# Optimization experiments

Hardware: AMD Instinct MI355X
Metric: run time of the kernel (lower is better)

Reference implementation:

```python
import jax, jax.numpy as jnp
import numpy as np

NUM_QUBITS = 12
BOND_DIM = 8
DIM = 2 ** NUM_QUBITS  # 4096


def setup_inputs() -> dict:
    key = jax.random.key(0)
    k0, k1, k2, k3 = jax.random.split(key, 4)
    core0 = jax.random.normal(k0, (2, BOND_DIM), dtype=jnp.float32) * 0.5
    cores_mid = jax.random.normal(k1, (NUM_QUBITS - 2, BOND_DIM, 2, BOND_DIM), dtype=jnp.float32) * 0.5
    core_last = jax.random.normal(k2, (BOND_DIM, 2), dtype=jnp.float32) * 0.5
    A = jax.random.normal(k3, (DIM, DIM), dtype=jnp.float32)
    H = 0.5 * (A + A.T)  # Hamiltonians are symmetric
    return {"core0": core0, "cores_mid": cores_mid, "core_last": core_last, "H": H}


def _build_state(core0, cores_mid, core_last):
    # Sequential MPS contraction: state grows (2^k, D) site by site.
    state = core0  # (2, D)
    n_mid = cores_mid.shape[0]
    D = core0.shape[1]
    for i in range(n_mid):  # fixed, small layer loop (not a data-dim loop)
        # (S, a) x (a, p, b) -> (S, p, b) -> (S*2, b)
        state = jnp.einsum('sa,apb->spb', state, cores_mid[i]).reshape(-1, D)
    # (S, a) x (a, p) -> flat state vector of length 2^n
    psi = jnp.einsum('sa,ap->sp', state, core_last).reshape(-1)
    return psi


def reference(core0, cores_mid, core_last, H):
    psi = _build_state(core0, cores_mid, core_last)  # (2^n,)
    norm = jnp.dot(psi, psi)
    hpsi = H @ psi
    energy = jnp.dot(psi, hpsi) / norm          # <psi|H|psi>/<psi|psi>
    e2 = jnp.dot(psi, H @ hpsi) / norm          # <psi|H^2|psi>/<psi|psi>
    variance = jnp.maximum(e2 - energy * energy, 0.0)
    return jnp.stack([energy, variance])
```

## Files before the change

kernel.cpp:

```cpp
#include <hip/hip_runtime.h>
#include <hip/hip_bf16.h>


#define DIM 4096
#define BOND 8
#define NMID 10
#define T 128
#define NT (DIM / T)
#define NPAIRS (NT * (NT + 1) / 2)


__global__ __launch_bounds__(256) void init_kernel(float* __restrict__ hpsi_g,
                                                   int* __restrict__ cnt) {
  const float4 z = {0.f, 0.f, 0.f, 0.f};
  reinterpret_cast<float4*>(hpsi_g)[blockIdx.x * 256 + threadIdx.x] = z;
  if (blockIdx.x == 0 && threadIdx.x == 0) *cnt = 0;
}

__global__ __launch_bounds__(256) void fused_kernel(
    const float* __restrict__ core0,
    const float* __restrict__ cores_mid,
    const float* __restrict__ core_last,
    const float* __restrict__ H,
    float* __restrict__ psi_g,
    float* __restrict__ hpsi_g,
    int* __restrict__ cnt,
    float* __restrict__ out) {
  __shared__ float c0[16], cm[NMID * 128], cl[16];
  __shared__ float xI[T], xJ[T], yI_s[T], yJp[4 * T];
  __shared__ double sred[12];
  __shared__ int s_old;

  int rem = blockIdx.x;
  int bi = 0;
  while (rem >= NT - bi) { rem -= (NT - bi); ++bi; }
  const int bj = bi + rem;
  const bool diag = (bi == bj);

  if (threadIdx.x < 16) {
    c0[threadIdx.x] = core0[threadIdx.x];
    cl[threadIdx.x] = core_last[threadIdx.x];
  }
  for (int j = threadIdx.x; j < NMID * 128; j += 256) cm[j] = cores_mid[j];
  __syncthreads();

  {
    const int local = threadIdx.x & 127;
    const int slice = (threadIdx.x < 128) ? bi : bj;
    const int idx = slice * T + local;

    float v[BOND], nv[BOND];
    const int s0 = (idx >> 11) & 1;
#pragma unroll
    for (int a = 0; a < BOND; a++) v[a] = c0[s0 * BOND + a];
#pragma unroll
    for (int i = 0; i < NMID; i++) {
      const int p = (idx >> (10 - i)) & 1;
      const float* M = &cm[i * 128 + p * BOND];
#pragma unroll
      for (int b = 0; b < BOND; b++) nv[b] = v[0] * M[b];
#pragma unroll
      for (int a = 1; a < BOND; a++) {
#pragma unroll
        for (int b = 0; b < BOND; b++) nv[b] += v[a] * M[a * 16 + b];
      }
#pragma unroll
      for (int a = 0; a < BOND; a++) v[a] = nv[a];
    }
    const int pl = idx & 1;
    float ps = 0.f;
#pragma unroll
    for (int a = 0; a < BOND; a++) ps += v[a] * cl[a * 2 + pl];

    if (threadIdx.x < 128) xI[local] = ps; else xJ[local] = ps;

    if (diag && threadIdx.x < 128) psi_g[idx] = ps;
  }
  __syncthreads();

  const int wave = threadIdx.x >> 6;
  const int lane = threadIdx.x & 63;
  const float* __restrict__ base = H + (size_t)(bi * T) * DIM + bj * T;

  float aJx = 0.f, aJy = 0.f;
  const float pJx = xJ[lane * 2], pJy = xJ[lane * 2 + 1];

#pragma unroll 4
  for (int k = 0; k < T / 4; ++k) {
    const int r = k * 4 + wave;
    const float2 a = *reinterpret_cast<const float2*>(base + (size_t)r * DIM + lane * 2);
    const float xr = xI[r];
    aJx += a.x * xr;
    aJy += a.y * xr;
    float d = a.x * pJx + a.y * pJy;
#pragma unroll
    for (int off = 32; off > 0; off >>= 1) d += __shfl_down(d, off, 64);
    if (lane == 0) yI_s[r] = d;
  }

  yJp[wave * T + lane * 2] = aJx;
  yJp[wave * T + lane * 2 + 1] = aJy;
  __syncthreads();

  if (threadIdx.x < T) {
    atomicAdd(&hpsi_g[bi * T + threadIdx.x], yI_s[threadIdx.x]);
    if (!diag) {
      const float yj = yJp[threadIdx.x] + yJp[T + threadIdx.x] +
                       yJp[2 * T + threadIdx.x] + yJp[3 * T + threadIdx.x];
      atomicAdd(&hpsi_g[bj * T + threadIdx.x], yj);
    }
  }
  __syncthreads();

  if (threadIdx.x == 0) {
    __threadfence();
    s_old = atomicAdd(cnt, 1);
  }
  __syncthreads();
  if (s_old == NPAIRS - 1) {
    __threadfence();
    double n = 0.0, ph = 0.0, hh = 0.0;
    for (int i = threadIdx.x; i < DIM; i += 256) {
      const float p = __hip_atomic_load(&psi_g[i], __ATOMIC_RELAXED,
                                        __HIP_MEMORY_SCOPE_AGENT);
      const float h = __hip_atomic_load(&hpsi_g[i], __ATOMIC_RELAXED,
                                        __HIP_MEMORY_SCOPE_AGENT);
      const double pd = (double)p, hd = (double)h;
      n += pd * pd;
      ph += pd * hd;
      hh += hd * hd;
    }
#pragma unroll
    for (int off = 32; off > 0; off >>= 1) {
      n += __shfl_down(n, off, 64);
      ph += __shfl_down(ph, off, 64);
      hh += __shfl_down(hh, off, 64);
    }
    if (lane == 0) { sred[wave] = n; sred[4 + wave] = ph; sred[8 + wave] = hh; }
    __syncthreads();
    if (threadIdx.x == 0) {
      double N = 0.0, P = 0.0, HH = 0.0;
#pragma unroll
      for (int w = 0; w < 4; w++) { N += sred[w]; P += sred[4 + w]; HH += sred[8 + w]; }
      const double e = P / N;
      const double e2 = HH / N;
      double var = e2 - e * e;
      if (var < 0.0) var = 0.0;
      out[0] = (float)e;
      out[1] = (float)var;
    }
  }
}

extern "C" void kernel_launch(void* const* d_in, const int* in_sizes, int n_in,
                              void* d_out, int out_size, void* d_ws, size_t ws_size,
                              hipStream_t stream) {
  const float* core0 = (const float*)d_in[0];
  const float* cores_mid = (const float*)d_in[1];
  const float* core_last = (const float*)d_in[2];
  const float* H = (const float*)d_in[3];

  float* psi = (float*)d_ws;
  float* hpsi = psi + DIM;
  int* cnt = (int*)(hpsi + DIM);

  init_kernel<<<4, 256, 0, stream>>>(hpsi, cnt);
  fused_kernel<<<NPAIRS, 256, 0, stream>>>(core0, cores_mid, core_last, H,
                                           psi, hpsi, cnt, (float*)d_out);
}
```

Before: 132.6 us.

## Precompute psi in init kernel and widen symv tile loads with LDS row reduction

```diff
diff --git a/kernel.cpp b/kernel.cpp
--- a/kernel.cpp
+++ b/kernel.cpp
@@ -10,24 +10,60 @@
 #define NPAIRS (NT * (NT + 1) / 2)
 
 
-__global__ __launch_bounds__(256) void init_kernel(float* __restrict__ hpsi_g,
-                                                   int* __restrict__ cnt) {
-  const float4 z = {0.f, 0.f, 0.f, 0.f};
-  reinterpret_cast<float4*>(hpsi_g)[blockIdx.x * 256 + threadIdx.x] = z;
-  if (blockIdx.x == 0 && threadIdx.x == 0) *cnt = 0;
-}
-
-__global__ __launch_bounds__(256) void fused_kernel(
+__global__ __launch_bounds__(256) void init_kernel(
     const float* __restrict__ core0,
     const float* __restrict__ cores_mid,
     const float* __restrict__ core_last,
+    float* __restrict__ psi_g,
+    float* __restrict__ hpsi_g,
+    int* __restrict__ cnt) {
+  __shared__ float c0[16], cm[NMID * 128], cl[16];
+
+  if (threadIdx.x < 16) {
+    c0[threadIdx.x] = core0[threadIdx.x];
+    cl[threadIdx.x] = core_last[threadIdx.x];
+  }
+  for (int j = threadIdx.x; j < NMID * 128; j += 256) cm[j] = cores_mid[j];
+  __syncthreads();
+
+  const int idx = blockIdx.x * 256 + threadIdx.x;
+  hpsi_g[idx] = 0.f;
+  if (idx == 0) *cnt = 0;
+
+  float v[BOND], nv[BOND];
+  const int s0 = (idx >> 11) & 1;
+#pragma unroll
+  for (int a = 0; a < BOND; a++) v[a] = c0[s0 * BOND + a];
+#pragma unroll
+  for (int i = 0; i < NMID; i++) {
+    const int p = (idx >> (10 - i)) & 1;
+    const float* M = &cm[i * 128 + p * BOND];
+#pragma unroll
+    for (int b = 0; b < BOND; b++) nv[b] = v[0] * M[b];
+#pragma unroll
+    for (int a = 1; a < BOND; a++) {
+#pragma unroll
+      for (int b = 0; b < BOND; b++) nv[b] += v[a] * M[a * 16 + b];
+    }
+#pragma unroll
+    for (int a = 0; a < BOND; a++) v[a] = nv[a];
+  }
+  const int pl = idx & 1;
+  float ps = 0.f;
+#pragma unroll
+  for (int a = 0; a < BOND; a++) ps += v[a] * cl[a * 2 + pl];
+  psi_g[idx] = ps;
+}
+
+__global__ __launch_bounds__(256) void symv_kernel(
     const float* __restrict__ H,
-    float* __restrict__ psi_g,
+    const float* __restrict__ psi_g,
     float* __restrict__ hpsi_g,
     int* __restrict__ cnt,
     float* __restrict__ out) {
-  __shared__ float c0[16], cm[NMID * 128], cl[16];
-  __shared__ float xI[T], xJ[T], yI_s[T], yJp[4 * T];
+  __shared__ float xI[T], xJ[T];
+  __shared__ float yIp[32 * 129];
+  __shared__ float yJp[8 * 128];
   __shared__ double sred[12];
   __shared__ int s_old;
 
@@ -37,78 +73,45 @@
   const int bj = bi + rem;
   const bool diag = (bi == bj);
 
-  if (threadIdx.x < 16) {
-    c0[threadIdx.x] = core0[threadIdx.x];
-    cl[threadIdx.x] = core_last[threadIdx.x];
-  }
-  for (int j = threadIdx.x; j < NMID * 128; j += 256) cm[j] = cores_mid[j];
-  __syncthreads();
-
-  {
-    const int local = threadIdx.x & 127;
-    const int slice = (threadIdx.x < 128) ? bi : bj;
-    const int idx = slice * T + local;
-
-    float v[BOND], nv[BOND];
-    const int s0 = (idx >> 11) & 1;
-#pragma unroll
-    for (int a = 0; a < BOND; a++) v[a] = c0[s0 * BOND + a];
-#pragma unroll
-    for (int i = 0; i < NMID; i++) {
-      const int p = (idx >> (10 - i)) & 1;
-      const float* M = &cm[i * 128 + p * BOND];
-#pragma unroll
-      for (int b = 0; b < BOND; b++) nv[b] = v[0] * M[b];
-#pragma unroll
-      for (int a = 1; a < BOND; a++) {
-#pragma unroll
-        for (int b = 0; b < BOND; b++) nv[b] += v[a] * M[a * 16 + b];
-      }
-#pragma unroll
-      for (int a = 0; a < BOND; a++) v[a] = nv[a];
-    }
-    const int pl = idx & 1;
-    float ps = 0.f;
-#pragma unroll
-    for (int a = 0; a < BOND; a++) ps += v[a] * cl[a * 2 + pl];
-
-    if (threadIdx.x < 128) xI[local] = ps; else xJ[local] = ps;
-
-    if (diag && threadIdx.x < 128) psi_g[idx] = ps;
-  }
+  if (threadIdx.x < T) xI[threadIdx.x] = psi_g[bi * T + threadIdx.x];
+  else xJ[threadIdx.x - T] = psi_g[bj * T + threadIdx.x - T];
   __syncthreads();
 
   const int wave = threadIdx.x >> 6;
   const int lane = threadIdx.x & 63;
+  const int half = lane >> 5;
+  const int l31 = lane & 31;
+  const int c = l31 * 4;
+
+  const float4 pj = *reinterpret_cast<const float4*>(&xJ[c]);
   const float* __restrict__ base = H + (size_t)(bi * T) * DIM + bj * T;
 
-  float aJx = 0.f, aJy = 0.f;
-  const float pJx = xJ[lane * 2], pJy = xJ[lane * 2 + 1];
-
-#pragma unroll 4
-  for (int k = 0; k < T / 4; ++k) {
-    const int r = k * 4 + wave;
-    const float2 a = *reinterpret_cast<const float2*>(base + (size_t)r * DIM + lane * 2);
+  float4 aJ = {0.f, 0.f, 0.f, 0.f};
+#pragma unroll
+  for (int k = 0; k < 16; ++k) {
+    const int r = k * 8 + wave * 2 + half;
+    const float4 a = *reinterpret_cast<const float4*>(base + (size_t)r * DIM + c);
     const float xr = xI[r];
-    aJx += a.x * xr;
-    aJy += a.y * xr;
-    float d = a.x * pJx + a.y * pJy;
-#pragma unroll
-    for (int off = 32; off > 0; off >>= 1) d += __shfl_down(d, off, 64);
-    if (lane == 0) yI_s[r] = d;
+    aJ.x += a.x * xr; aJ.y += a.y * xr; aJ.z += a.z * xr; aJ.w += a.w * xr;
+    yIp[l31 * 129 + r] = a.x * pj.x + a.y * pj.y + a.z * pj.z + a.w * pj.w;
   }
-
-  yJp[wave * T + lane * 2] = aJx;
-  yJp[wave * T + lane * 2 + 1] = aJy;
+  *reinterpret_cast<float4*>(&yJp[(wave * 2 + half) * 128 + c]) = aJ;
   __syncthreads();
 
-  if (threadIdx.x < T) {
-    atomicAdd(&hpsi_g[bi * T + threadIdx.x], yI_s[threadIdx.x]);
-    if (!diag) {
-      const float yj = yJp[threadIdx.x] + yJp[T + threadIdx.x] +
-                       yJp[2 * T + threadIdx.x] + yJp[3 * T + threadIdx.x];
-      atomicAdd(&hpsi_g[bj * T + threadIdx.x], yj);
-    }
+  {
+    const int r = threadIdx.x >> 1;
+    const int h = threadIdx.x & 1;
+    float s = 0.f;
+#pragma unroll
+    for (int i = 0; i < 16; ++i) s += yIp[(16 * h + i) * 129 + r];
+    s += __shfl_down(s, 1, 64);
+    if (h == 0) atomicAdd(&hpsi_g[bi * T + r], s);
+  }
+  if (!diag && threadIdx.x < T) {
+    float s = 0.f;
+#pragma unroll
+    for (int q = 0; q < 8; ++q) s += yJp[q * 128 + threadIdx.x];
+    atomicAdd(&hpsi_g[bj * T + threadIdx.x], s);
   }
   __syncthreads();
 
@@ -164,7 +167,6 @@
   float* hpsi = psi + DIM;
   int* cnt = (int*)(hpsi + DIM);
 
-  init_kernel<<<4, 256, 0, stream>>>(hpsi, cnt);
-  fused_kernel<<<NPAIRS, 256, 0, stream>>>(core0, cores_mid, core_last, H,
-                                           psi, hpsi, cnt, (float*)d_out);
+  init_kernel<<<DIM / 256, 256, 0, stream>>>(core0, cores_mid, core_last, psi, hpsi, cnt);
+  symv_kernel<<<NPAIRS, 256, 0, stream>>>(H, psi, hpsi, cnt, (float*)d_out);
 }
```

Measured after the change: 124.7 us. -6.0%, faster.
